# Kernel tuning notes

Measured on AMD Instinct MI355X. Metric: run time of the kernel, lower is better.

## Reference

```python
import jax, jax.numpy as jnp
import numpy as np

EPS = float(np.finfo(float).eps)
NUM_RFS = 1

def conv3d(x, w):
    # x: [N,C,D,H,W], w: [O,I,kd,kh,kw], VALID, stride 1 (matches F.conv3d defaults)
    return jax.lax.conv_general_dilated(
        x, w, window_strides=(1, 1, 1), padding='VALID',
        dimension_numbers=('NCDHW', 'OIDHW', 'NCDHW'))

def setup_inputs() -> dict:
    key = jax.random.key(0)
    k1, k2, k3, k4 = jax.random.split(key, 4)
    x = jax.random.normal(k1, (1, 1, 3, 394, 394), jnp.float32)
    x_prev = jax.random.normal(k2, (1, 1, 3, 394, 394), jnp.float32)
    # params stored post-permute as [out_ch, in_ch, kt, kh, kw]
    filts_temp = jax.random.normal(k3, (16, 1, 3, 11, 11), jnp.float32)
    filts_notemp = jax.random.normal(k4, (16, 1, 1, 11, 11), jnp.float32)
    return {"x": x, "x_prev": x_prev, "filts_temp": filts_temp, "filts_notemp": filts_notemp}

def reference(x, x_prev, filts_temp, filts_notemp):
    corr_x = NUM_RFS * filts_temp.shape[3]  # kh
    corr_y = NUM_RFS * filts_temp.shape[4]  # kw
    num_filts = filts_temp.shape[0] + filts_notemp.shape[0]

    def feats(v):
        vt = jax.nn.relu(conv3d(v, filts_temp)) / 2           # [1,16,1,H',W'] (T==kt)
        vn = jax.nn.relu(conv3d(v[:, :, -1:, :, :], filts_notemp))  # last frame, [1,16,1,H',W']
        return jnp.concatenate([vt, vn], axis=1)              # [1,32,1,H',W']

    f = feats(x)
    fp = feats(x_prev)
    # channel-wise normalization
    x1 = f / (jnp.sum(f, axis=1, keepdims=True) + EPS)
    x1_prev = fp / (jnp.sum(fp, axis=1, keepdims=True) + EPS)

    y_max, x_max = x1.shape[3], x1.shape[4]
    yc = y_max - 2 * corr_y
    xc = x_max - 2 * corr_x
    # cropped current-frame channels become conv filters: [nf,1,1,yc,xc]
    x1_filts = x1[:, :, :, corr_y:y_max - corr_y, corr_x:x_max - corr_x].reshape(
        num_filts, 1, 1, yc, xc)
    prev = x1_prev.reshape(1, 1, num_filts, y_max, x_max)
    # normalized cross-correlation via conv3d: out [1, nf, nf, 2cy+1, 2cx+1]
    x2 = conv3d(prev, x1_filts)
    x2 = x2.reshape(1, num_filts, num_filts, 2 * corr_y + 1, 2 * corr_x + 1)
    x2 = x2 / ((y_max - 2 * corr_y) * (x_max - 2 * corr_y))  # faithful to original (uses corr_y twice)
    return x1, x2
```

## Files before the change

kernel.cpp:

```cpp
#include <hip/hip_runtime.h>
#include <hip/hip_bf16.h>


typedef unsigned short ushort_t;
typedef unsigned int uint_t;
typedef unsigned char uchar_t;
typedef __attribute__((ext_vector_type(4))) float f32x4;
typedef __attribute__((ext_vector_type(16))) float f32x16;
typedef __attribute__((ext_vector_type(4))) uint_t uint4_t;
typedef __attribute__((ext_vector_type(2))) uint_t uint2_t;
typedef __attribute__((ext_vector_type(8))) int int8v;

#define EPSF 2.2204460492503131e-16f
#define X1_N (32*384*384)
#define X2_N (32*32*23*23)

#define FILTB_ROW_B 12288
#define FILTB_BYTES (372*48*32*8)
#define PREVB_STRIDE 432
#define PREVB_BYTES (32*385*PREVB_STRIDE)
#define ZERO_BYTES ((size_t)FILTB_BYTES + PREVB_BYTES)
#define FT2_ELEMS (16*45*12)

#define YMAX 367
#define NCHUNKS 16
#define INV_AREA (1.0f/131044.0f)

#define SB_COPY_B 432
#define SB_DYB_B  (8*SB_COPY_B)
#define SB_ROW_B  (4*SB_DYB_B)
#define SB_BYTES  (2*2*SB_ROW_B)

#define SA_BYTES  (8*FILTB_ROW_B)
#define SMEM_TOTAL (SA_BYTES + SB_BYTES)

__device__ __forceinline__ uint_t f32_to_e4m3(float f) {
  if (f < 0.015625f)
    return (uint_t)__float2int_rn(f * 512.0f);
  uint_t b = __builtin_bit_cast(uint_t, f);
  int e = (int)(b >> 23) - 127;
  uint_t m = b & 0x7FFFFFu;
  uint_t keep = m >> 20;
  uint_t rest = m & 0xFFFFFu;
  keep += (rest > 0x80000u) || (rest == 0x80000u && (keep & 1u));
  if (keep == 8u) { keep = 0u; e += 1; }
  if (e > 8) return 0x7Eu;
  return (uint_t)(((e + 7) << 3) | keep);
}

__global__ void prep_kernel(const float* __restrict__ ft, const float* __restrict__ fn,
                            float* __restrict__ fT2)
{
  const int e = blockIdx.x * 256 + threadIdx.x;
  if (e < FT2_ELEMS) {
    const int chp = e / 540;
    const int rem = e - chp * 540;
    const int row = rem / 12;
    const int j = rem - row * 12;
    float v = 0.f;
    if (j < 11) {
      if (row < 33)      v = ft[chp * 363 + row * 11 + j];
      else if (row < 44) v = fn[chp * 121 + (row - 33) * 11 + j];
    }
    fT2[e] = v;
  }
}

__global__ __launch_bounds__(128, 4) void feat_kernel(
    const float* __restrict__ xcur, const float* __restrict__ xprev,
    const float* __restrict__ fT2,
    float* __restrict__ out_x1, uchar_t* __restrict__ prevb)
{
  __shared__ float sPx[3 * 18 * 28];
  __shared__ float sOut[32][9][20];
  const int tid = threadIdx.x;
  const int chp = tid & 15;
  const int r = tid >> 4;
  const int j0 = blockIdx.x * 16;
  const int i0 = blockIdx.y * 8;
  const int i = i0 + r;
  const int mode = blockIdx.z;
  const float* __restrict__ xin = mode ? xprev : xcur;

  for (int e = tid; e < 3 * 18 * 26; e += 128) {
    const int t = e / 468;
    const int rem = e - t * 468;
    const int ri = rem / 26;
    const int ci = rem - ri * 26;
    sPx[(t * 18 + ri) * 28 + ci] = xin[((size_t)t * 394 + i0 + ri) * 394 + j0 + ci];
  }
  __syncthreads();

  const float* __restrict__ fbase = fT2 + chp * 540;

  float accT[16], accN[16];
#pragma unroll
  for (int p = 0; p < 16; ++p) { accT[p] = 0.f; accN[p] = 0.f; }

#pragma unroll
  for (int t = 0; t < 3; ++t) {
    for (int a = 0; a < 11; ++a) {
      const float* row = &sPx[(t * 18 + r + a) * 28];
      float wv[26];
#pragma unroll
      for (int k = 0; k < 6; ++k) {
        const f32x4 q = *(const f32x4*)(row + 4 * k);
        wv[4 * k + 0] = q[0]; wv[4 * k + 1] = q[1];
        wv[4 * k + 2] = q[2]; wv[4 * k + 3] = q[3];
      }
      wv[24] = row[24]; wv[25] = row[25];

      const float* fr = fbase + (t * 11 + a) * 12;
      const f32x4 fq0 = *(const f32x4*)(fr);
      const f32x4 fq1 = *(const f32x4*)(fr + 4);
      const f32x4 fq2 = *(const f32x4*)(fr + 8);
      float fv[12];
#pragma unroll
      for (int k = 0; k < 4; ++k) { fv[k] = fq0[k]; fv[4+k] = fq1[k]; fv[8+k] = fq2[k]; }
      float fv2[12];
      if (t == 2) {
        const float* fr2 = fbase + (33 + a) * 12;
        const f32x4 g0 = *(const f32x4*)(fr2);
        const f32x4 g1 = *(const f32x4*)(fr2 + 4);
        const f32x4 g2 = *(const f32x4*)(fr2 + 8);
#pragma unroll
        for (int k = 0; k < 4; ++k) { fv2[k] = g0[k]; fv2[4+k] = g1[k]; fv2[8+k] = g2[k]; }
      }

#pragma unroll
      for (int b = 0; b < 11; ++b) {
        const float fT = fv[b];
#pragma unroll
        for (int p = 0; p < 16; ++p) accT[p] = fmaf(wv[b + p], fT, accT[p]);
        if (t == 2) {
          const float fN = fv2[b];
#pragma unroll
          for (int p = 0; p < 16; ++p) accN[p] = fmaf(wv[b + p], fN, accN[p]);
        }
      }
    }
  }

  float o0[16], o1[16];
#pragma unroll
  for (int p = 0; p < 16; ++p) {
    const float vT = fmaxf(accT[p], 0.f) * 0.5f;
    const float vN = fmaxf(accN[p], 0.f);
    float s = vT + vN;
    s += __shfl_xor(s, 1);  s += __shfl_xor(s, 2);
    s += __shfl_xor(s, 4);  s += __shfl_xor(s, 8);
    const float inv = 1.f / (s + EPSF);
    o0[p] = vT * inv;
    o1[p] = vN * inv;
  }

  if (mode == 0) {
#pragma unroll
    for (int p = 0; p < 16; ++p) {
      sOut[chp][r][p] = o0[p];
      sOut[chp + 16][r][p] = o1[p];
    }
    __syncthreads();
#pragma unroll
    for (int it = 0; it < 8; ++it) {
      const int idx = it * 128 + tid;
      const int seg = idx & 3;
      const int rr = (idx >> 2) & 7;
      const int chn = idx >> 5;
      const f32x4 v = {sOut[chn][rr][4 * seg], sOut[chn][rr][4 * seg + 1],
                       sOut[chn][rr][4 * seg + 2], sOut[chn][rr][4 * seg + 3]};
      *(f32x4*)(out_x1 + (size_t)chn * 147456 + (i0 + rr) * 384 + j0 + 4 * seg) = v;
    }
  } else {
    uint4_t u0, u1;
#pragma unroll
    for (int q = 0; q < 4; ++q) {
      u0[q] = f32_to_e4m3(o0[4*q]) | (f32_to_e4m3(o0[4*q+1]) << 8) |
              (f32_to_e4m3(o0[4*q+2]) << 16) | (f32_to_e4m3(o0[4*q+3]) << 24);
      u1[q] = f32_to_e4m3(o1[4*q]) | (f32_to_e4m3(o1[4*q+1]) << 8) |
              (f32_to_e4m3(o1[4*q+2]) << 16) | (f32_to_e4m3(o1[4*q+3]) << 24);
    }
    *(uint4_t*)(prevb + ((size_t)chp * 385 + i) * PREVB_STRIDE + j0) = u0;
    *(uint4_t*)(prevb + ((size_t)(chp + 16) * 385 + i) * PREVB_STRIDE + j0) = u1;
  }
}

__global__ __launch_bounds__(256) void pack_kernel(
    const float* __restrict__ x1, uchar_t* __restrict__ filtb)
{
  const int e = blockIdx.x * 256 + threadIdx.x;
  if (e >= 362 * 46 * 32) return;
  const int o = e & 31;
  const int q = e >> 5;
  const int xb = q % 46;
  const int rowr = q / 46 + 5;
  const int i = rowr + 6;
  const int j0 = 11 + xb * 8;
  const float* src = x1 + (size_t)o * 147456 + i * 384 + j0;
  uint_t w0 = 0, w1 = 0;
#pragma unroll
  for (int k = 0; k < 4; ++k) {
    w0 |= f32_to_e4m3((j0 + k     <= 372) ? src[k]     : 0.f) << (8 * k);
    w1 |= f32_to_e4m3((j0 + 4 + k <= 372) ? src[4 + k] : 0.f) << (8 * k);
  }
  uint2_t u = {w0, w1};
  const int off = (xb >> 3) * 2048 + ((xb >> 1) & 1) * 1024 +
                  ((xb >> 2) & 1) * 512 + o * 16 + (xb & 1) * 8;
  *(uint2_t*)(filtb + (size_t)rowr * FILTB_ROW_B + off) = u;
}

__global__ __launch_bounds__(1024, 4) void corr_kernel(
    const uchar_t* __restrict__ filtb, const uchar_t* __restrict__ prevb,
    float* __restrict__ x2)
{
  extern __shared__ uchar_t smem[];

  const int tid = threadIdx.x;
  const int lane = tid & 63;
  const int wv = tid >> 6;
  const bool is_comp = (wv < 12);
  const int pw = wv - 12;
  const int cgu = is_comp ? ((wv >= 6) ? 1 : 0) : (pw >> 1);
  const int w = is_comp ? (wv - 6 * ((wv >= 6) ? 1 : 0)) : 0;
  const int kg = lane >> 5;
  const int nn = lane & 31;

  const int chpair = blockIdx.x / NCHUNKS;
  const int chunk = blockIdx.x % NCHUNKS;
  const int ch = 2 * chpair + cgu;
  const int y0 = (chunk * YMAX) / NCHUNKS;
  const int y1 = ((chunk + 1) * YMAX) / NCHUNKS;

  uint_t* const sBg = (uint_t*)(smem + SA_BYTES) + cgu * (2 * (SB_ROW_B / 4));

  int boffB[3];
#pragma unroll
  for (int nt = 0; nt < 3; ++nt) {
    const int n = nt * 32 + nn;
    const int dyb = n / 24;
    const int dxr = n - 24 * dyb;
    const int dx = (dxr < 23) ? dxr : 22;
    const int s = dx & 7;
    boffB[nt] = dyb * SB_DYB_B + s * SB_COPY_B + (dx >> 3) * 8 + kg * 32;
  }

  const int tl = is_comp ? 0 : ((pw & 1) * 64 + lane);
  const bool b_act = (!is_comp) && (tl < 104);
  const int sdyb = b_act ? (tl / 26) : 0;
  const int sg = tl - 26 * (b_act ? (tl / 26) : 0);
  const uchar_t* srcbase = prevb + ((size_t)(ch * 385 + 6 * sdyb)) * PREVB_STRIDE;
  const int dstoff = sdyb * (SB_DYB_B / 4) + 4 * sg;

  auto stage_B = [&](int yy, int buf) {
    const uint_t* sw = (const uint_t*)(srcbase + (size_t)yy * PREVB_STRIDE) + 4 * sg;
    const uint4_t lo = *(const uint4_t*)(sw);
    const uint2_t hi = *(const uint2_t*)(sw + 4);
    const uint_t wd[6] = {lo.x, lo.y, lo.z, lo.w, hi.x, hi.y};
    uint_t* dst = sBg + buf * (SB_ROW_B / 4) + dstoff;
#pragma unroll
    for (int s = 0; s < 8; ++s) {
      const int off = s >> 2;
      const int b = (s & 3) * 8;
      uint4_t v;
      if (b == 0) {
        v = uint4_t{wd[off], wd[off + 1], wd[off + 2], wd[off + 3]};
      } else {
        v = uint4_t{(wd[off]     >> b) | (wd[off + 1] << (32 - b)),
                    (wd[off + 1] >> b) | (wd[off + 2] << (32 - b)),
                    (wd[off + 2] >> b) | (wd[off + 3] << (32 - b)),
                    (wd[off + 3] >> b) | (wd[off + 4] << (32 - b))};
      }
      *(uint4_t*)(dst + s * (SB_COPY_B / 4)) = v;
    }
  };

  const int ptid = is_comp ? 0 : (pw * 64 + lane);
  auto stage_A = [&](int row, int slot) {
    const uchar_t* src = filtb + (size_t)row * FILTB_ROW_B + ptid * 48;
    uchar_t* dst = smem + (size_t)slot * FILTB_ROW_B + ptid * 48;
    const uint4_t v0 = *(const uint4_t*)(src);
    const uint4_t v1 = *(const uint4_t*)(src + 16);
    const uint4_t v2 = *(const uint4_t*)(src + 32);
    *(uint4_t*)(dst) = v0;
    *(uint4_t*)(dst + 16) = v1;
    *(uint4_t*)(dst + 32) = v2;
  };

  f32x16 acc[3];
#pragma unroll
  for (int nt = 0; nt < 3; ++nt)
#pragma unroll
    for (int r = 0; r < 16; ++r) acc[nt][r] = 0.f;

  if (!is_comp) {
#pragma unroll
    for (int r6 = 0; r6 < 6; ++r6)
      stage_A(y0 + r6, (y0 + r6) & 7);
    if (b_act) stage_B(y0, 0);
  }
  __syncthreads();

  for (int y = y0; y < y1; ++y) {
    const int pb = (y - y0) & 1;

    if (is_comp) {
      const char* sBrd = (const char*)sBg + pb * SB_ROW_B;
      const char* aRow = (const char*)smem +
          ((y + 5 - w) & 7) * FILTB_ROW_B + kg * 512 + nn * 16;

      __builtin_amdgcn_s_setprio(1);
#pragma unroll 1
      for (int kt = 0; kt < 6; ++kt) {
        const char* ap = aRow + (kt << 11);
        const uint4_t a0 = *(const uint4_t*)(ap);
        const uint4_t a1 = *(const uint4_t*)(ap + 1024);
        const int8v Af = {(int)a0.x, (int)a0.y, (int)a0.z, (int)a0.w,
                          (int)a1.x, (int)a1.y, (int)a1.z, (int)a1.w};
#pragma unroll
        for (int nt = 0; nt < 3; ++nt) {
          const char* bp = sBrd + boffB[nt] + (kt << 6);
          const uint2_t b0 = *(const uint2_t*)(bp);
          const uint2_t b1 = *(const uint2_t*)(bp + 8);
          const uint2_t b2 = *(const uint2_t*)(bp + 16);
          const uint2_t b3 = *(const uint2_t*)(bp + 24);
          const int8v Bf = {(int)b0.x, (int)b0.y, (int)b1.x, (int)b1.y,
                            (int)b2.x, (int)b2.y, (int)b3.x, (int)b3.y};
          acc[nt] = __builtin_amdgcn_mfma_scale_f32_32x32x64_f8f6f4(
              Af, Bf, acc[nt], 0, 0,
              0, 0x7F7F7F7F, 0, 0x7F7F7F7F);
        }
      }
      __builtin_amdgcn_s_setprio(0);
    } else {
      if (b_act && y + 1 < y1) stage_B(y + 1, pb ^ 1);
      if (y + 6 <= y1 + 4) stage_A(y + 6, (y + 6) & 7);
    }

    __syncthreads();
  }

  if (is_comp) {
#pragma unroll
    for (int nt = 0; nt < 3; ++nt) {
      const int n = nt * 32 + nn;
      const int dyb = n / 24;
      const int dxr = n - 24 * dyb;
      if (dxr < 23) {
        const int dy = w + 6 * dyb;
        if (dy <= 22) {
#pragma unroll
          for (int r = 0; r < 16; ++r) {
            const int o = (r & 3) + 8 * (r >> 2) + 4 * kg;
            atomicAdd(&x2[((o * 32 + ch) * 23 + dy) * 23 + dxr],
                      acc[nt][r] * INV_AREA);
          }
        }
      }
    }
  }
}

extern "C" void kernel_launch(void* const* d_in, const int* in_sizes, int n_in,
                              void* d_out, int out_size, void* d_ws, size_t ws_size,
                              hipStream_t stream)
{
  const float* x     = (const float*)d_in[0];
  const float* xprev = (const float*)d_in[1];
  const float* ft    = (const float*)d_in[2];
  const float* fn    = (const float*)d_in[3];
  float* out = (float*)d_out;

  uchar_t* filtb = (uchar_t*)d_ws;
  uchar_t* prevb = filtb + FILTB_BYTES;
  float* fT2 = (float*)(prevb + PREVB_BYTES);

  static bool attr_set = false;
  if (!attr_set) {
    (void)hipFuncSetAttribute((const void*)corr_kernel,
        hipFuncAttributeMaxDynamicSharedMemorySize, SMEM_TOTAL);
    attr_set = true;
  }

  hipMemsetAsync(d_ws, 0, ZERO_BYTES, stream);
  hipMemsetAsync(out + X1_N, 0, (size_t)X2_N * sizeof(float), stream);

  prep_kernel<<<dim3((FT2_ELEMS + 255) / 256), 256, 0, stream>>>(ft, fn, fT2);
  feat_kernel<<<dim3(24, 48, 2), 128, 0, stream>>>(x, xprev, fT2, out, prevb);
  pack_kernel<<<dim3((362 * 46 * 32 + 255) / 256), 256, 0, stream>>>(out, filtb);
  corr_kernel<<<dim3(16 * NCHUNKS), 1024, SMEM_TOTAL, stream>>>(
      filtb, prevb, out + X1_N);
}
```

Measured before the change: 276.1 us.

## Fuse filter packing into feature kernel and fold memsets into prep kernel

Removes the separate pack_kernel: the feature kernel now writes the e4m3-quantized, swizzled filter bytes directly while computing x1, so x1 is no longer re-read from global memory. The two hipMemsetAsync calls are replaced by zeroing loops inside the prep kernel, which cuts the launch count. The trade-off is scattered single-byte stores from the feature kernel, which may coalesce poorly. The prep kernel now also has to zero several MB on its own.

```diff
diff --git a/kernel.cpp b/kernel.cpp
--- a/kernel.cpp
+++ b/kernel.cpp
@@ -21,6 +21,10 @@
 #define PREVB_BYTES (32*385*PREVB_STRIDE)
 #define ZERO_BYTES ((size_t)FILTB_BYTES + PREVB_BYTES)
 #define FT2_ELEMS (16*45*12)
+
+#define ZERO16 (ZERO_BYTES / 16)
+#define X2Z16  ((X2_N * 4) / 16)
+#define PREP_WORK (ZERO16 + X2Z16 + FT2_ELEMS)
 
 #define YMAX 367
 #define NCHUNKS 16
@@ -49,12 +53,18 @@
 }
 
 __global__ void prep_kernel(const float* __restrict__ ft, const float* __restrict__ fn,
-                            float* __restrict__ fT2)
+                            float* __restrict__ fT2, uchar_t* __restrict__ wsz,
+                            float* __restrict__ x2)
 {
-  const int e = blockIdx.x * 256 + threadIdx.x;
-  if (e < FT2_ELEMS) {
-    const int chp = e / 540;
-    const int rem = e - chp * 540;
+  const long e = (long)blockIdx.x * 256 + threadIdx.x;
+  if (e < (long)ZERO16) {
+    ((uint4_t*)wsz)[e] = uint4_t{0u, 0u, 0u, 0u};
+  } else if (e < (long)(ZERO16 + X2Z16)) {
+    ((uint4_t*)x2)[e - ZERO16] = uint4_t{0u, 0u, 0u, 0u};
+  } else if (e < (long)PREP_WORK) {
+    const int e2 = (int)(e - ZERO16 - X2Z16);
+    const int chp = e2 / 540;
+    const int rem = e2 - chp * 540;
     const int row = rem / 12;
     const int j = rem - row * 12;
     float v = 0.f;
@@ -62,14 +72,15 @@
       if (row < 33)      v = ft[chp * 363 + row * 11 + j];
       else if (row < 44) v = fn[chp * 121 + (row - 33) * 11 + j];
     }
-    fT2[e] = v;
+    fT2[e2] = v;
   }
 }
 
 __global__ __launch_bounds__(128, 4) void feat_kernel(
     const float* __restrict__ xcur, const float* __restrict__ xprev,
     const float* __restrict__ fT2,
-    float* __restrict__ out_x1, uchar_t* __restrict__ prevb)
+    float* __restrict__ out_x1, uchar_t* __restrict__ prevb,
+    uchar_t* __restrict__ filtb)
 {
   __shared__ float sPx[3 * 18 * 28];
   __shared__ float sOut[32][9][20];
@@ -155,6 +166,21 @@
   }
 
   if (mode == 0) {
+    if (i >= 11 && i <= 372) {
+      uchar_t* const rowbase = filtb + (size_t)(i - 6) * FILTB_ROW_B;
+#pragma unroll
+      for (int p = 0; p < 16; ++p) {
+        const int c = j0 + p;
+        if (c >= 11 && c <= 372) {
+          const int cb = c - 11;
+          const int xb = cb >> 3;
+          const int off = (xb >> 3) * 2048 + ((xb >> 1) & 1) * 1024 +
+                          ((xb >> 2) & 1) * 512 + (xb & 1) * 8 + (cb & 7);
+          rowbase[off + chp * 16]        = (uchar_t)f32_to_e4m3(o0[p]);
+          rowbase[off + (chp + 16) * 16] = (uchar_t)f32_to_e4m3(o1[p]);
+        }
+      }
+    }
 #pragma unroll
     for (int p = 0; p < 16; ++p) {
       sOut[chp][r][p] = o0[p];
@@ -183,30 +209,6 @@
     *(uint4_t*)(prevb + ((size_t)chp * 385 + i) * PREVB_STRIDE + j0) = u0;
     *(uint4_t*)(prevb + ((size_t)(chp + 16) * 385 + i) * PREVB_STRIDE + j0) = u1;
   }
-}
-
-__global__ __launch_bounds__(256) void pack_kernel(
-    const float* __restrict__ x1, uchar_t* __restrict__ filtb)
-{
-  const int e = blockIdx.x * 256 + threadIdx.x;
-  if (e >= 362 * 46 * 32) return;
-  const int o = e & 31;
-  const int q = e >> 5;
-  const int xb = q % 46;
-  const int rowr = q / 46 + 5;
-  const int i = rowr + 6;
-  const int j0 = 11 + xb * 8;
-  const float* src = x1 + (size_t)o * 147456 + i * 384 + j0;
-  uint_t w0 = 0, w1 = 0;
-#pragma unroll
-  for (int k = 0; k < 4; ++k) {
-    w0 |= f32_to_e4m3((j0 + k     <= 372) ? src[k]     : 0.f) << (8 * k);
-    w1 |= f32_to_e4m3((j0 + 4 + k <= 372) ? src[4 + k] : 0.f) << (8 * k);
-  }
-  uint2_t u = {w0, w1};
-  const int off = (xb >> 3) * 2048 + ((xb >> 1) & 1) * 1024 +
-                  ((xb >> 2) & 1) * 512 + o * 16 + (xb & 1) * 8;
-  *(uint2_t*)(filtb + (size_t)rowr * FILTB_ROW_B + off) = u;
 }
 
 __global__ __launch_bounds__(1024, 4) void corr_kernel(
@@ -381,12 +383,10 @@
     attr_set = true;
   }
 
-  hipMemsetAsync(d_ws, 0, ZERO_BYTES, stream);
-  hipMemsetAsync(out + X1_N, 0, (size_t)X2_N * sizeof(float), stream);
-
-  prep_kernel<<<dim3((FT2_ELEMS + 255) / 256), 256, 0, stream>>>(ft, fn, fT2);
-  feat_kernel<<<dim3(24, 48, 2), 128, 0, stream>>>(x, xprev, fT2, out, prevb);
-  pack_kernel<<<dim3((362 * 46 * 32 + 255) / 256), 256, 0, stream>>>(out, filtb);
+  prep_kernel<<<dim3((PREP_WORK + 255) / 256), 256, 0, stream>>>(
+      ft, fn, fT2, (uchar_t*)d_ws, out + X1_N);
+  feat_kernel<<<dim3(24, 48, 2), 128, 0, stream>>>(
+      x, xprev, fT2, out, prevb, filtb);
   corr_kernel<<<dim3(16 * NCHUNKS), 1024, SMEM_TOTAL, stream>>>(
       filtb, prevb, out + X1_N);
 }
```

After: 261.1 us. 5.5% less time.
